# Kernel optimization log

Measured on AMD Instinct MI355X. Metric: run time of the kernel, lower is better.

## Reference

```python
import jax, jax.numpy as jnp
import numpy as np

B, S, D, H = 4, 2048, 1024, 16
DK = D // H

def setup_inputs() -> dict:
    key = jax.random.key(0)
    ks = jax.random.split(key, 7)
    f = lambda k, shape: jax.random.normal(k, shape, dtype=jnp.float32)
    return {
        "query": f(ks[0], (B, S, D)),
        "key":   f(ks[1], (B, S, D)),
        "value": f(ks[2], (B, S, D)),
        "w_q": f(ks[3], (D, D)) * (D ** -0.5),
        "w_k": f(ks[4], (D, D)) * (D ** -0.5),
        "w_v": f(ks[5], (D, D)) * (D ** -0.5),
        "w_o": f(ks[6], (D, D)) * (D ** -0.5),
    }

def reference(query, key, value, w_q, w_k, w_v, w_o):
    # Linear layers: y = x @ W^T (torch nn.Linear convention), bias=False
    def split_heads(x):  # [B,S,D] -> [B,H,S,DK]
        return x.reshape(B, S, H, DK).transpose(0, 2, 1, 3)
    Q = split_heads(query @ w_q.T)
    K = split_heads(key @ w_k.T)
    V = split_heads(value @ w_v.T)
    scale = jnp.float32(1.0 / np.sqrt(DK))
    scores = jnp.einsum('bhqd,bhkd->bhqk', Q, K) * scale  # [B,H,Sq,Sk]
    attn = jax.nn.softmax(scores, axis=-1)
    out = jnp.einsum('bhqk,bhkd->bhqd', attn, V)  # [B,H,Sq,DK]
    out = out.transpose(0, 2, 1, 3).reshape(B, S, D)
    return out @ w_o.T
```

## Files before the change

### kernel.cpp

```cpp
#include <hip/hip_runtime.h>
#include <stdint.h>

#define NB 4
#define NS 2048
#define ND 1024
#define NH 16
#define NDK 64
#define NM (NB*NS)

typedef __attribute__((ext_vector_type(8))) short short8;
typedef __attribute__((ext_vector_type(8))) unsigned short ushort8v;
typedef __attribute__((ext_vector_type(4))) unsigned short ushort4v;
typedef __attribute__((ext_vector_type(4))) float f32x4;
typedef __attribute__((ext_vector_type(16))) float f32x16;

__device__ __forceinline__ unsigned short f2bf(float f) {
  union { float f; uint32_t u; } v; v.f = f;
  uint32_t u = v.u;
  return (unsigned short)((u + 0x7FFFu + ((u >> 16) & 1u)) >> 16);
}

__device__ __forceinline__ void gload16(const void* g, void* l) {
  __builtin_amdgcn_global_load_lds(
      (const __attribute__((address_space(1))) void*)g,
      (__attribute__((address_space(3))) void*)l, 16, 0, 0);
}

__device__ __forceinline__ int xcd_swz(int flat, int nwg) {
  return (flat & 7) * (nwg >> 3) + (flat >> 3);
}

__global__ void convert_all(
    const float* __restrict__ x0, const float* __restrict__ x1, const float* __restrict__ x2,
    const float* __restrict__ w0, const float* __restrict__ w1,
    const float* __restrict__ w2, const float* __restrict__ w3,
    unsigned short* __restrict__ ox0, unsigned short* __restrict__ ox1, unsigned short* __restrict__ ox2,
    unsigned short* __restrict__ ow0, unsigned short* __restrict__ ow1,
    unsigned short* __restrict__ ow2, unsigned short* __restrict__ ow3)
{
  const float* src;
  unsigned short* dst;
  size_t i;
  if (blockIdx.y < 3) {
    src = blockIdx.y == 0 ? x0 : (blockIdx.y == 1 ? x1 : x2);
    dst = blockIdx.y == 0 ? ox0 : (blockIdx.y == 1 ? ox1 : ox2);
    i = ((size_t)blockIdx.x * 256 + threadIdx.x) * 8;
  } else {
    if (blockIdx.x >= 2048) return;
    size_t e = ((size_t)blockIdx.x * 256 + threadIdx.x) * 8;
    int which = (int)(e >> 20);
    size_t off = e & ((1u << 20) - 1);
    const float* ws[4] = {w0, w1, w2, w3};
    unsigned short* wd[4] = {ow0, ow1, ow2, ow3};
    src = ws[which]; dst = wd[which]; i = off;
  }
  f32x4 a = *(const f32x4*)(src + i);
  f32x4 b = *(const f32x4*)(src + i + 4);
  ushort8v h;
  h[0]=f2bf(a.x); h[1]=f2bf(a.y); h[2]=f2bf(a.z); h[3]=f2bf(a.w);
  h[4]=f2bf(b.x); h[5]=f2bf(b.y); h[6]=f2bf(b.z); h[7]=f2bf(b.w);
  *(ushort8v*)(dst + i) = h;
}

#define GPHASE(MH, NH, LA, LB)                                                 \
  {                                                                            \
    if (LA) {                                                                  \
      _Pragma("unroll") for (int mm = 0; mm < 4; ++mm)                         \
        _Pragma("unroll") for (int kk = 0; kk < 2; ++kk)                       \
          af[mm][kk] = *(const short8*)(Ab + (MH)*8192 + mm*2048 + rowb + aoff[kk]); \
    }                                                                          \
    if (LB) {                                                                  \
      _Pragma("unroll") for (int nn = 0; nn < 2; ++nn)                         \
        _Pragma("unroll") for (int kk = 0; kk < 2; ++kk)                       \
          bf[nn][kk] = *(const short8*)(Bb + (NH)*4096 + nn*2048 + rowb + aoff[kk]); \
    }                                                                          \
    __builtin_amdgcn_s_barrier();                                              \
    __builtin_amdgcn_s_setprio(1);                                             \
    _Pragma("unroll") for (int mm = 0; mm < 4; ++mm)                           \
      _Pragma("unroll") for (int nn = 0; nn < 2; ++nn)                         \
        _Pragma("unroll") for (int kk = 0; kk < 2; ++kk)                       \
          acc[(MH)*4+mm][(NH)*2+nn] = __builtin_amdgcn_mfma_f32_16x16x32_bf16( \
              af[mm][kk], bf[nn][kk], acc[(MH)*4+mm][(NH)*2+nn], 0, 0, 0);     \
    __builtin_amdgcn_s_setprio(0);                                             \
    __builtin_amdgcn_s_barrier();                                              \
  }

template<int OUT, int PRESCALE>
__device__ __forceinline__ void gemm256_core(
    const unsigned short* __restrict__ A,
    const unsigned short* __restrict__ Bt,
    void* __restrict__ Cout,
    unsigned short* lds, int m0, int n0)
{
  const int K = ND, N = ND;
  const int tid = threadIdx.x;
  const int lane = tid & 63, wid = tid >> 6;
  const int l15 = lane & 15, lg = lane >> 4;
  const int wr = wid >> 2, wc = wid & 3;
  const float QSC = 0.125f * 1.44269504088896f;

  const unsigned short* Asrc[4];
  const unsigned short* Bsrc[4];
#pragma unroll
  for (int l = 0; l < 4; ++l) {
    int cidx = l*512 + tid;
    int r = cidx >> 3;
    int cs = ((cidx & 7) ^ (r & 7)) * 8;
    Asrc[l] = A  + (size_t)(m0 + r)*K + cs;
    Bsrc[l] = Bt + (size_t)(n0 + r)*K + cs;
  }

  const int rowb = l15 * 128;
  int aoff[2];
  aoff[0] = ((lg)     ^ (l15 & 7)) * 16;
  aoff[1] = ((4 + lg) ^ (l15 & 7)) * 16;

  f32x4 acc[8][4] = {};
  short8 af[4][2], bf[2][2];

#pragma unroll
  for (int l = 0; l < 4; ++l) {
    gload16(Asrc[l], lds + l*4096 + tid*8);
    gload16(Bsrc[l], lds + 16384 + l*4096 + tid*8);
  }
  asm volatile("s_waitcnt vmcnt(0)" ::: "memory");
  __builtin_amdgcn_s_barrier();

  const int NT = K / 64;
  for (int t = 0; t < NT; ++t) {
    const int cur = t & 1;
    if (t + 1 < NT) {
      unsigned short* dstA = lds + (cur^1)*32768;
#pragma unroll
      for (int l = 0; l < 4; ++l) {
        gload16(Asrc[l] + (t+1)*64, dstA + l*4096 + tid*8);
        gload16(Bsrc[l] + (t+1)*64, dstA + 16384 + l*4096 + tid*8);
      }
    }
    const char* Ab = (const char*)(lds + cur*32768) + wr*16384;
    const char* Bb = (const char*)(lds + cur*32768 + 16384) + (wc>>1)*16384 + (wc&1)*8192;

    GPHASE(0, 0, 1, 1)
    GPHASE(0, 1, 0, 1)
    GPHASE(1, 1, 1, 0)
    GPHASE(1, 0, 0, 1)

    asm volatile("s_waitcnt vmcnt(0)" ::: "memory");
    __builtin_amdgcn_s_barrier();
  }

#pragma unroll
  for (int m = 0; m < 8; ++m)
#pragma unroll
    for (int n = 0; n < 4; ++n)
#pragma unroll
      for (int i = 0; i < 4; ++i) {
        int row = m0 + wr*128 + m*16 + lg*4 + i;
        int col = n0 + wc*64 + n*16 + l15;
        float val = PRESCALE ? acc[m][n][i] * QSC : acc[m][n][i];
        if (OUT == 0)
          ((float*)Cout)[(size_t)row * N + col] = val;
        else if (OUT == 1)
          ((unsigned short*)Cout)[(size_t)row * N + col] = f2bf(val);
        else
          ((unsigned short*)Cout)[((size_t)((row >> 11)*1024 + col))*NS + (row & (NS-1))]
              = f2bf(val);
      }
}

__global__ __launch_bounds__(512, 2) void gemm_qkv(
    const unsigned short* __restrict__ Xq, const unsigned short* __restrict__ Wq, unsigned short* Qb,
    const unsigned short* __restrict__ Xk, const unsigned short* __restrict__ Wk, unsigned short* Kb,
    const unsigned short* __restrict__ Xv, const unsigned short* __restrict__ Wv, unsigned short* VbT)
{
  __shared__ unsigned short lds[65536];
  int flat = (blockIdx.z * 32 + blockIdx.y) * 4 + blockIdx.x;
  int swz = xcd_swz(flat, 384);
  int z = swz >> 7, rem = swz & 127;
  int m0 = (rem >> 2) * 256, n0 = (rem & 3) * 256;
  if (z == 0)      gemm256_core<1,1>(Xq, Wq, Qb,  lds, m0, n0);
  else if (z == 1) gemm256_core<1,0>(Xk, Wk, Kb,  lds, m0, n0);
  else             gemm256_core<2,0>(Xv, Wv, VbT, lds, m0, n0);
}

__global__ __launch_bounds__(512, 2) void gemm_o(
    const unsigned short* __restrict__ A, const unsigned short* __restrict__ Bt, float* C)
{
  __shared__ unsigned short lds[65536];
  int flat = blockIdx.y * 4 + blockIdx.x;
  int swz = xcd_swz(flat, 128);
  gemm256_core<0,0>(A, Bt, C, lds, (swz >> 2) * 256, (swz & 3) * 256);
}

__global__ __launch_bounds__(256, 4) void flash_attn(
    const unsigned short* __restrict__ Qb,
    const unsigned short* __restrict__ Kb,
    const unsigned short* __restrict__ VT,
    unsigned short* __restrict__ O)
{
  __shared__ unsigned short Kt[2][64*64];
  __shared__ unsigned short Vt[2][64*64];
  const int tid = threadIdx.x, lane = tid & 63, wid = tid >> 6;
  const int l31 = lane & 31, hi = lane >> 5;
  int flat = blockIdx.y * 16 + blockIdx.x;
  int swz = xcd_swz(flat, 1024);
  const int bh = swz >> 4, b = bh >> 4, h = bh & 15;
  const int q0 = (swz & 15) * 128 + wid * 32;

  const unsigned short* Kp[2]; const unsigned short* Vp[2]; int dofs[2];
#pragma unroll
  for (int p = 0; p < 2; ++p) {
    int slot = tid + p*256;
    int g = slot >> 6, r = slot & 63;
    Kp[p] = Kb + ((size_t)(b*NS + r))*ND + h*64 + g*8;
    Vp[p] = VT + ((size_t)(bh*64 + r))*NS + g*8;
    dofs[p] = slot * 8;
  }

  short8 qf[4];
#pragma unroll
  for (int ks = 0; ks < 4; ++ks)
    qf[ks] = *(const short8*)(Qb + (size_t)(b*NS + q0 + l31)*ND + h*64 + ks*16 + hi*8);

  f32x16 oacc[2] = {};
  float lsum = 0.f;

#pragma unroll
  for (int p = 0; p < 2; ++p) {
    gload16(Kp[p], &Kt[0][dofs[p]]);
    gload16(Vp[p], &Vt[0][dofs[p]]);
  }
  __syncthreads();

  for (int t = 0; t < NS/64; ++t) {
    const int cur = t & 1;
    if (t + 1 < NS/64) {
#pragma unroll
      for (int p = 0; p < 2; ++p) {
        gload16(Kp[p] + (size_t)(t+1)*64*ND, &Kt[cur^1][dofs[p]]);
        gload16(Vp[p] + (t+1)*64,            &Vt[cur^1][dofs[p]]);
      }
    }
    const char* Kc = (const char*)Kt[cur];
    const char* Vc = (const char*)Vt[cur];

    f32x16 st[2] = {};
    __builtin_amdgcn_s_setprio(1);
#pragma unroll
    for (int n = 0; n < 2; ++n) {
      const int r = n*32 + l31;
#pragma unroll
      for (int ks = 0; ks < 4; ++ks) {
        short8 kf = *(const short8*)(Kc + (((2*ks + hi) << 10) + r*16));
        st[n] = __builtin_amdgcn_mfma_f32_32x32x16_bf16(kf, qf[ks], st[n], 0, 0, 0);
      }
    }
    __builtin_amdgcn_s_setprio(0);

    float rs = 0.f;
#pragma unroll
    for (int n = 0; n < 2; ++n)
#pragma unroll
      for (int r = 0; r < 16; ++r) {
        float p = __builtin_amdgcn_exp2f(st[n][r]);
        st[n][r] = p;
        rs += p;
      }
    rs += __shfl_xor(rs, 32);
    lsum += rs;

    uint32_t w[2][4][2];
#pragma unroll
    for (int n = 0; n < 2; ++n)
#pragma unroll
      for (int e = 0; e < 4; ++e) {
        asm("v_cvt_pk_bf16_f32 %0, %1, %2"
            : "=v"(w[n][e][0]) : "v"(st[n][4*e+0]), "v"(st[n][4*e+1]));
        asm("v_cvt_pk_bf16_f32 %0, %1, %2"
            : "=v"(w[n][e][1]) : "v"(st[n][4*e+2]), "v"(st[n][4*e+3]));
      }

    short8 pa[2][2];
#pragma unroll
    for (int n = 0; n < 2; ++n)
#pragma unroll
      for (int ksl = 0; ksl < 2; ++ksl) {
        uint32_t a0 = w[n][2*ksl][0], b0 = w[n][2*ksl+1][0];
        uint32_t a1 = w[n][2*ksl][1], b1 = w[n][2*ksl+1][1];
        asm("v_permlane32_swap_b32 %0, %1" : "+v"(a0), "+v"(b0));
        asm("v_permlane32_swap_b32 %0, %1" : "+v"(a1), "+v"(b1));
        union { uint32_t u[4]; short8 s; } f;
        f.u[0] = a0; f.u[1] = a1; f.u[2] = b0; f.u[3] = b1;
        pa[n][ksl] = f.s;
      }

    __builtin_amdgcn_s_setprio(1);
#pragma unroll
    for (int d = 0; d < 2; ++d) {
      const int dr = d*32 + l31;
#pragma unroll
      for (int n = 0; n < 2; ++n)
#pragma unroll
        for (int ksl = 0; ksl < 2; ++ksl) {
          const int g = n*4 + ksl*2 + hi;
          short8 vf = *(const short8*)(Vc + ((g << 10) + dr*16));
          oacc[d] = __builtin_amdgcn_mfma_f32_32x32x16_bf16(pa[n][ksl], vf, oacc[d], 0, 0, 0);
        }
    }
    __builtin_amdgcn_s_setprio(0);
    __syncthreads();
  }

  float linv[16];
#pragma unroll
  for (int r = 0; r < 16; ++r)
    linv[r] = 1.0f / __shfl(lsum, (r & 3) + 8*(r >> 2) + 4*hi);
#pragma unroll
  for (int d = 0; d < 2; ++d)
#pragma unroll
    for (int r = 0; r < 16; ++r) {
      int qrow = q0 + (r & 3) + 8*(r >> 2) + 4*hi;
      O[(size_t)(b*NS + qrow)*ND + h*64 + d*32 + l31] = f2bf(oacc[d][r] * linv[r]);
    }
}

extern "C" void kernel_launch(void* const* d_in, const int* in_sizes, int n_in,
                              void* d_out, int out_size, void* d_ws, size_t ws_size,
                              hipStream_t stream) {
  const float* q  = (const float*)d_in[0];
  const float* k  = (const float*)d_in[1];
  const float* v  = (const float*)d_in[2];
  const float* wq = (const float*)d_in[3];
  const float* wk = (const float*)d_in[4];
  const float* wv = (const float*)d_in[5];
  const float* wo = (const float*)d_in[6];

  unsigned short* Wq = (unsigned short*)d_ws;
  unsigned short* Wk = Wq + (size_t)ND*ND;
  unsigned short* Wv = Wk + (size_t)ND*ND;
  unsigned short* Wo = Wv + (size_t)ND*ND;
  unsigned short* Xq = Wo + (size_t)ND*ND;
  unsigned short* Xk = Xq + (size_t)NM*ND;
  unsigned short* Xv = Xk + (size_t)NM*ND;
  unsigned short* Qb = Xv + (size_t)NM*ND;
  unsigned short* Kb = Qb + (size_t)NM*ND;
  unsigned short* VbT = (unsigned short*)d_out;
  unsigned short* Ob  = Xq;

  convert_all<<<dim3(NM*ND/(256*8), 4), 256, 0, stream>>>(
      q, k, v, wq, wk, wv, wo, Xq, Xk, Xv, Wq, Wk, Wv, Wo);

  gemm_qkv<<<dim3(4, 32, 3), 512, 0, stream>>>(Xq, Wq, Qb, Xk, Wk, Kb, Xv, Wv, VbT);

  flash_attn<<<dim3(16, 64), 256, 0, stream>>>(Qb, Kb, VbT, Ob);

  gemm_o<<<dim3(4, 32), 512, 0, stream>>>(Ob, Wo, (float*)d_out);
}
```

Measured before the change: 220.0 us.

## Process 64 query rows per wave in attention and narrow output GEMM tiles

The flash attention kernel now gives each wave two 32-row query sub-tiles. Each K/V tile loaded into LDS is therefore reused for twice as many query rows, and the grid is halved. The output projection GEMM is made templated on tile width and uses 256x128 tiles, which doubles its block count from 128 to 256 to fill more CUs. In exchange, attention needs more registers and runs at lower occupancy (launch bounds drop from 4 to 2 blocks per CU), and fewer attention blocks may leave some CUs less busy.

```diff
diff --git a/kernel.cpp b/kernel.cpp
--- a/kernel.cpp
+++ b/kernel.cpp
@@ -70,22 +70,22 @@
           af[mm][kk] = *(const short8*)(Ab + (MH)*8192 + mm*2048 + rowb + aoff[kk]); \
     }                                                                          \
     if (LB) {                                                                  \
-      _Pragma("unroll") for (int nn = 0; nn < 2; ++nn)                         \
+      _Pragma("unroll") for (int nn = 0; nn < NN; ++nn)                        \
         _Pragma("unroll") for (int kk = 0; kk < 2; ++kk)                       \
-          bf[nn][kk] = *(const short8*)(Bb + (NH)*4096 + nn*2048 + rowb + aoff[kk]); \
+          bf[nn][kk] = *(const short8*)(Bb + (NH)*(NN*2048) + nn*2048 + rowb + aoff[kk]); \
     }                                                                          \
     __builtin_amdgcn_s_barrier();                                              \
     __builtin_amdgcn_s_setprio(1);                                             \
     _Pragma("unroll") for (int mm = 0; mm < 4; ++mm)                           \
-      _Pragma("unroll") for (int nn = 0; nn < 2; ++nn)                         \
+      _Pragma("unroll") for (int nn = 0; nn < NN; ++nn)                        \
         _Pragma("unroll") for (int kk = 0; kk < 2; ++kk)                       \
-          acc[(MH)*4+mm][(NH)*2+nn] = __builtin_amdgcn_mfma_f32_16x16x32_bf16( \
-              af[mm][kk], bf[nn][kk], acc[(MH)*4+mm][(NH)*2+nn], 0, 0, 0);     \
+          acc[(MH)*4+mm][(NH)*NN+nn] = __builtin_amdgcn_mfma_f32_16x16x32_bf16( \
+              af[mm][kk], bf[nn][kk], acc[(MH)*4+mm][(NH)*NN+nn], 0, 0, 0);    \
     __builtin_amdgcn_s_setprio(0);                                             \
     __builtin_amdgcn_s_barrier();                                              \
   }
 
-template<int OUT, int PRESCALE>
+template<int OUT, int PRESCALE, int BN>
 __device__ __forceinline__ void gemm256_core(
     const unsigned short* __restrict__ A,
     const unsigned short* __restrict__ Bt,
@@ -93,6 +93,9 @@
     unsigned short* lds, int m0, int n0)
 {
   const int K = ND, N = ND;
+  const int NN = BN / 128;
+  const int NBL = BN / 64;
+  const int ASZ = 16384, BSZ = BN * 64, SZ = ASZ + BSZ;
   const int tid = threadIdx.x;
   const int lane = tid & 63, wid = tid >> 6;
   const int l15 = lane & 15, lg = lane >> 4;
@@ -100,13 +103,19 @@
   const float QSC = 0.125f * 1.44269504088896f;
 
   const unsigned short* Asrc[4];
-  const unsigned short* Bsrc[4];
+  const unsigned short* Bsrc[NBL];
 #pragma unroll
   for (int l = 0; l < 4; ++l) {
     int cidx = l*512 + tid;
     int r = cidx >> 3;
     int cs = ((cidx & 7) ^ (r & 7)) * 8;
-    Asrc[l] = A  + (size_t)(m0 + r)*K + cs;
+    Asrc[l] = A + (size_t)(m0 + r)*K + cs;
+  }
+#pragma unroll
+  for (int l = 0; l < NBL; ++l) {
+    int cidx = l*512 + tid;
+    int r = cidx >> 3;
+    int cs = ((cidx & 7) ^ (r & 7)) * 8;
     Bsrc[l] = Bt + (size_t)(n0 + r)*K + cs;
   }
 
@@ -115,14 +124,13 @@
   aoff[0] = ((lg)     ^ (l15 & 7)) * 16;
   aoff[1] = ((4 + lg) ^ (l15 & 7)) * 16;
 
-  f32x4 acc[8][4] = {};
-  short8 af[4][2], bf[2][2];
-
-#pragma unroll
-  for (int l = 0; l < 4; ++l) {
-    gload16(Asrc[l], lds + l*4096 + tid*8);
-    gload16(Bsrc[l], lds + 16384 + l*4096 + tid*8);
-  }
+  f32x4 acc[8][2*NN] = {};
+  short8 af[4][2], bf[NN][2];
+
+#pragma unroll
+  for (int l = 0; l < 4; ++l) gload16(Asrc[l], lds + l*4096 + tid*8);
+#pragma unroll
+  for (int l = 0; l < NBL; ++l) gload16(Bsrc[l], lds + ASZ + l*4096 + tid*8);
   asm volatile("s_waitcnt vmcnt(0)" ::: "memory");
   __builtin_amdgcn_s_barrier();
 
@@ -130,15 +138,14 @@
   for (int t = 0; t < NT; ++t) {
     const int cur = t & 1;
     if (t + 1 < NT) {
-      unsigned short* dstA = lds + (cur^1)*32768;
-#pragma unroll
-      for (int l = 0; l < 4; ++l) {
-        gload16(Asrc[l] + (t+1)*64, dstA + l*4096 + tid*8);
-        gload16(Bsrc[l] + (t+1)*64, dstA + 16384 + l*4096 + tid*8);
-      }
-    }
-    const char* Ab = (const char*)(lds + cur*32768) + wr*16384;
-    const char* Bb = (const char*)(lds + cur*32768 + 16384) + (wc>>1)*16384 + (wc&1)*8192;
+      unsigned short* dst = lds + (cur^1)*SZ;
+#pragma unroll
+      for (int l = 0; l < 4; ++l) gload16(Asrc[l] + (t+1)*64, dst + l*4096 + tid*8);
+#pragma unroll
+      for (int l = 0; l < NBL; ++l) gload16(Bsrc[l] + (t+1)*64, dst + ASZ + l*4096 + tid*8);
+    }
+    const char* Ab = (const char*)(lds + cur*SZ) + wr*16384;
+    const char* Bb = (const char*)(lds + cur*SZ + ASZ) + wc*(BN*32);
 
     GPHASE(0, 0, 1, 1)
     GPHASE(0, 1, 0, 1)
@@ -152,11 +159,11 @@
 #pragma unroll
   for (int m = 0; m < 8; ++m)
 #pragma unroll
-    for (int n = 0; n < 4; ++n)
+    for (int n = 0; n < 2*NN; ++n)
 #pragma unroll
       for (int i = 0; i < 4; ++i) {
         int row = m0 + wr*128 + m*16 + lg*4 + i;
-        int col = n0 + wc*64 + n*16 + l15;
+        int col = n0 + wc*(BN/4) + n*16 + l15;
         float val = PRESCALE ? acc[m][n][i] * QSC : acc[m][n][i];
         if (OUT == 0)
           ((float*)Cout)[(size_t)row * N + col] = val;
@@ -178,21 +185,21 @@
   int swz = xcd_swz(flat, 384);
   int z = swz >> 7, rem = swz & 127;
   int m0 = (rem >> 2) * 256, n0 = (rem & 3) * 256;
-  if (z == 0)      gemm256_core<1,1>(Xq, Wq, Qb,  lds, m0, n0);
-  else if (z == 1) gemm256_core<1,0>(Xk, Wk, Kb,  lds, m0, n0);
-  else             gemm256_core<2,0>(Xv, Wv, VbT, lds, m0, n0);
+  if (z == 0)      gemm256_core<1,1,256>(Xq, Wq, Qb,  lds, m0, n0);
+  else if (z == 1) gemm256_core<1,0,256>(Xk, Wk, Kb,  lds, m0, n0);
+  else             gemm256_core<2,0,256>(Xv, Wv, VbT, lds, m0, n0);
 }
 
 __global__ __launch_bounds__(512, 2) void gemm_o(
     const unsigned short* __restrict__ A, const unsigned short* __restrict__ Bt, float* C)
 {
-  __shared__ unsigned short lds[65536];
-  int flat = blockIdx.y * 4 + blockIdx.x;
-  int swz = xcd_swz(flat, 128);
-  gemm256_core<0,0>(A, Bt, C, lds, (swz >> 2) * 256, (swz & 3) * 256);
-}
-
-__global__ __launch_bounds__(256, 4) void flash_attn(
+  __shared__ unsigned short lds[49152];
+  int flat = blockIdx.y * 8 + blockIdx.x;
+  int swz = xcd_swz(flat, 256);
+  gemm256_core<0,0,128>(A, Bt, C, lds, (swz >> 3) * 256, (swz & 7) * 128);
+}
+
+__global__ __launch_bounds__(256, 2) void flash_attn(
     const unsigned short* __restrict__ Qb,
     const unsigned short* __restrict__ Kb,
     const unsigned short* __restrict__ VT,
@@ -202,10 +209,10 @@
   __shared__ unsigned short Vt[2][64*64];
   const int tid = threadIdx.x, lane = tid & 63, wid = tid >> 6;
   const int l31 = lane & 31, hi = lane >> 5;
-  int flat = blockIdx.y * 16 + blockIdx.x;
-  int swz = xcd_swz(flat, 1024);
-  const int bh = swz >> 4, b = bh >> 4, h = bh & 15;
-  const int q0 = (swz & 15) * 128 + wid * 32;
+  int flat = blockIdx.y * 8 + blockIdx.x;
+  int swz = xcd_swz(flat, 512);
+  const int bh = swz >> 3, b = bh >> 4, h = bh & 15;
+  const int q0 = (swz & 7) * 256 + wid * 64;
 
   const unsigned short* Kp[2]; const unsigned short* Vp[2]; int dofs[2];
 #pragma unroll
@@ -217,13 +224,15 @@
     dofs[p] = slot * 8;
   }
 
-  short8 qf[4];
-#pragma unroll
-  for (int ks = 0; ks < 4; ++ks)
-    qf[ks] = *(const short8*)(Qb + (size_t)(b*NS + q0 + l31)*ND + h*64 + ks*16 + hi*8);
-
-  f32x16 oacc[2] = {};
-  float lsum = 0.f;
+  short8 qf[2][4];
+#pragma unroll
+  for (int qs = 0; qs < 2; ++qs)
+#pragma unroll
+    for (int ks = 0; ks < 4; ++ks)
+      qf[qs][ks] = *(const short8*)(Qb + (size_t)(b*NS + q0 + qs*32 + l31)*ND + h*64 + ks*16 + hi*8);
+
+  f32x16 oacc[2][2] = {};
+  float lsum[2] = {0.f, 0.f};
 
 #pragma unroll
   for (int p = 0; p < 2; ++p) {
@@ -244,55 +253,56 @@
     const char* Kc = (const char*)Kt[cur];
     const char* Vc = (const char*)Vt[cur];
 
-    f32x16 st[2] = {};
-    __builtin_amdgcn_s_setprio(1);
+    short8 pa[2][2][2];
+    float rs[2] = {0.f, 0.f};
+
 #pragma unroll
     for (int n = 0; n < 2; ++n) {
+      f32x16 st[2] = {};
       const int r = n*32 + l31;
+      __builtin_amdgcn_s_setprio(1);
 #pragma unroll
       for (int ks = 0; ks < 4; ++ks) {
         short8 kf = *(const short8*)(Kc + (((2*ks + hi) << 10) + r*16));
-        st[n] = __builtin_amdgcn_mfma_f32_32x32x16_bf16(kf, qf[ks], st[n], 0, 0, 0);
-      }
-    }
-    __builtin_amdgcn_s_setprio(0);
-
-    float rs = 0.f;
-#pragma unroll
-    for (int n = 0; n < 2; ++n)
-#pragma unroll
-      for (int r = 0; r < 16; ++r) {
-        float p = __builtin_amdgcn_exp2f(st[n][r]);
-        st[n][r] = p;
-        rs += p;
-      }
-    rs += __shfl_xor(rs, 32);
-    lsum += rs;
-
-    uint32_t w[2][4][2];
-#pragma unroll
-    for (int n = 0; n < 2; ++n)
-#pragma unroll
-      for (int e = 0; e < 4; ++e) {
-        asm("v_cvt_pk_bf16_f32 %0, %1, %2"
-            : "=v"(w[n][e][0]) : "v"(st[n][4*e+0]), "v"(st[n][4*e+1]));
-        asm("v_cvt_pk_bf16_f32 %0, %1, %2"
-            : "=v"(w[n][e][1]) : "v"(st[n][4*e+2]), "v"(st[n][4*e+3]));
-      }
-
-    short8 pa[2][2];
-#pragma unroll
-    for (int n = 0; n < 2; ++n)
-#pragma unroll
-      for (int ksl = 0; ksl < 2; ++ksl) {
-        uint32_t a0 = w[n][2*ksl][0], b0 = w[n][2*ksl+1][0];
-        uint32_t a1 = w[n][2*ksl][1], b1 = w[n][2*ksl+1][1];
-        asm("v_permlane32_swap_b32 %0, %1" : "+v"(a0), "+v"(b0));
-        asm("v_permlane32_swap_b32 %0, %1" : "+v"(a1), "+v"(b1));
-        union { uint32_t u[4]; short8 s; } f;
-        f.u[0] = a0; f.u[1] = a1; f.u[2] = b0; f.u[3] = b1;
-        pa[n][ksl] = f.s;
-      }
+        st[0] = __builtin_amdgcn_mfma_f32_32x32x16_bf16(kf, qf[0][ks], st[0], 0, 0, 0);
+        st[1] = __builtin_amdgcn_mfma_f32_32x32x16_bf16(kf, qf[1][ks], st[1], 0, 0, 0);
+      }
+      __builtin_amdgcn_s_setprio(0);
+#pragma unroll
+      for (int qs = 0; qs < 2; ++qs) {
+        float lrs = 0.f;
+#pragma unroll
+        for (int e = 0; e < 16; ++e) {
+          float p = __builtin_amdgcn_exp2f(st[qs][e]);
+          st[qs][e] = p;
+          lrs += p;
+        }
+        rs[qs] += lrs;
+        uint32_t w[4][2];
+#pragma unroll
+        for (int e = 0; e < 4; ++e) {
+          asm("v_cvt_pk_bf16_f32 %0, %1, %2"
+              : "=v"(w[e][0]) : "v"(st[qs][4*e+0]), "v"(st[qs][4*e+1]));
+          asm("v_cvt_pk_bf16_f32 %0, %1, %2"
+              : "=v"(w[e][1]) : "v"(st[qs][4*e+2]), "v"(st[qs][4*e+3]));
+        }
+#pragma unroll
+        for (int ksl = 0; ksl < 2; ++ksl) {
+          uint32_t a0 = w[2*ksl][0], b0 = w[2*ksl+1][0];
+          uint32_t a1 = w[2*ksl][1], b1 = w[2*ksl+1][1];
+          asm("v_permlane32_swap_b32 %0, %1" : "+v"(a0), "+v"(b0));
+          asm("v_permlane32_swap_b32 %0, %1" : "+v"(a1), "+v"(b1));
+          union { uint32_t u[4]; short8 s; } f;
+          f.u[0] = a0; f.u[1] = a1; f.u[2] = b0; f.u[3] = b1;
+          pa[qs][n][ksl] = f.s;
+        }
+      }
+    }
+#pragma unroll
+    for (int qs = 0; qs < 2; ++qs) {
+      rs[qs] += __shfl_xor(rs[qs], 32);
+      lsum[qs] += rs[qs];
+    }
 
     __builtin_amdgcn_s_setprio(1);
 #pragma unroll
@@ -304,24 +314,28 @@
         for (int ksl = 0; ksl < 2; ++ksl) {
           const int g = n*4 + ksl*2 + hi;
           short8 vf = *(const short8*)(Vc + ((g << 10) + dr*16));
-          oacc[d] = __builtin_amdgcn_mfma_f32_32x32x16_bf16(pa[n][ksl], vf, oacc[d], 0, 0, 0);
+          oacc[0][d] = __builtin_amdgcn_mfma_f32_32x32x16_bf16(pa[0][n][ksl], vf, oacc[0][d], 0, 0, 0);
+          oacc[1][d] = __builtin_amdgcn_mfma_f32_32x32x16_bf16(pa[1][n][ksl], vf, oacc[1][d], 0, 0, 0);
         }
     }
     __builtin_amdgcn_s_setprio(0);
     __syncthreads();
   }
 
-  float linv[16];
-#pragma unroll
-  for (int r = 0; r < 16; ++r)
-    linv[r] = 1.0f / __shfl(lsum, (r & 3) + 8*(r >> 2) + 4*hi);
-#pragma unroll
-  for (int d = 0; d < 2; ++d)
-#pragma unroll
-    for (int r = 0; r < 16; ++r) {
-      int qrow = q0 + (r & 3) + 8*(r >> 2) + 4*hi;
-      O[(size_t)(b*NS + qrow)*ND + h*64 + d*32 + l31] = f2bf(oacc[d][r] * linv[r]);
-    }
+#pragma unroll
+  for (int qs = 0; qs < 2; ++qs) {
+    float linv[16];
+#pragma unroll
+    for (int r = 0; r < 16; ++r)
+      linv[r] = 1.0f / __shfl(lsum[qs], (r & 3) + 8*(r >> 2) + 4*hi);
+#pragma unroll
+    for (int d = 0; d < 2; ++d)
+#pragma unroll
+      for (int r = 0; r < 16; ++r) {
+        int qrow = q0 + qs*32 + (r & 3) + 8*(r >> 2) + 4*hi;
+        O[(size_t)(b*NS + qrow)*ND + h*64 + d*32 + l31] = f2bf(oacc[qs][d][r] * linv[r]);
+      }
+  }
 }
 
 extern "C" void kernel_launch(void* const* d_in, const int* in_sizes, int n_in,
@@ -352,7 +366,7 @@
 
   gemm_qkv<<<dim3(4, 32, 3), 512, 0, stream>>>(Xq, Wq, Qb, Xk, Wk, Kb, Xv, Wv, VbT);
 
-  flash_attn<<<dim3(16, 64), 256, 0, stream>>>(Qb, Kb, VbT, Ob);
-
-  gemm_o<<<dim3(4, 32), 512, 0, stream>>>(Ob, Wo, (float*)d_out);
-}
+  flash_attn<<<dim3(8, 64), 256, 0, stream>>>(Qb, Kb, VbT, Ob);
+
+  gemm_o<<<dim3(8, 32), 512, 0, stream>>>(Ob, Wo, (float*)d_out);
+}
```

Result: faster. 205.7 us (-6.5%).
